# Optimization experiments

Hardware: AMD Instinct MI355X
Metric: run time of the kernel (lower is better)

The kernel has to match this reference:

```python
import jax, jax.numpy as jnp
import numpy as np

B, OBS, H, N = 16384, 512, 1024, 9

def setup_inputs() -> dict:
    key = jax.random.key(0)
    ks = jax.random.split(key, 12)
    s = 0.02
    return {
        "obs": jax.random.normal(ks[0], (B, OBS), jnp.float32),
        "agent_positions": jax.random.normal(ks[1], (B, N, 3), jnp.float32),
        "W1": jax.random.normal(ks[2], (OBS, H), jnp.float32) * s,
        "b1": jnp.zeros((H,), jnp.float32),
        "W2": jax.random.normal(ks[3], (H, H), jnp.float32) * s,
        "b2": jnp.zeros((H,), jnp.float32),
        "Wc1": jax.random.normal(ks[4], (H, H // 2), jnp.float32) * s,
        "bc1": jnp.zeros((H // 2,), jnp.float32),
        "Wc2": jax.random.normal(ks[5], (H // 2, 1), jnp.float32) * s,
        "bc2": jnp.zeros((1,), jnp.float32),
        "Wt1": jax.random.normal(ks[6], (H, H // 2), jnp.float32) * s,
        "bt1": jnp.zeros((H // 2,), jnp.float32),
        "Wt2": jax.random.normal(ks[7], (H // 2, 1), jnp.float32) * s,
        "bt2": jnp.zeros((1,), jnp.float32),
        "Wk1": jax.random.normal(ks[8], (2 * H, H), jnp.float32) * s,
        "bk1": jnp.zeros((H,), jnp.float32),
        "Wk2": jax.random.normal(ks[9], (H, 1), jnp.float32) * s,
        "bk2": jnp.zeros((1,), jnp.float32),
    }


def reference(obs, agent_positions, W1, b1, W2, b2, Wc1, bc1, Wc2, bc2,
              Wt1, bt1, Wt2, bt2, Wk1, bk1, Wk2, bk2):
    # global features: Linear->ReLU->Linear->ReLU
    g = jax.nn.relu(obs @ W1 + b1)
    g = jax.nn.relu(g @ W2 + b2)  # [B, H]

    # Each per-agent head is applied to the SAME g in the original loop,
    # so one pass + broadcast is mathematically identical.
    cov = jax.nn.sigmoid(jax.nn.relu(g @ Wc1 + bc1) @ Wc2 + bc2)  # [B,1]
    trk = jax.nn.sigmoid(jax.nn.relu(g @ Wt1 + bt1) @ Wt2 + bt2)  # [B,1]
    coop_in = jnp.concatenate([g, g], axis=-1)                    # [B,2H]
    coop = jax.nn.sigmoid(jax.nn.relu(coop_in @ Wk1 + bk1) @ Wk2 + bk2)  # [B,1]
    # mean over 8 identical cooperation scores == the score itself

    coverage = jnp.broadcast_to(cov, (cov.shape[0], N))      # [B, N]
    tracking = jnp.broadcast_to(trk, (trk.shape[0], N))      # [B, N]
    cooperation = jnp.broadcast_to(coop, (coop.shape[0], N)) # [B, N]
    return (coverage, tracking, cooperation)
```

## Files before the change

### kernel.cpp

```cpp
#include <hip/hip_runtime.h>
#include <hip/hip_bf16.h>

#define B_ROWS 16384
#define OBS_D  512
#define H_D    1024
#define N_AG   9

typedef __attribute__((ext_vector_type(8))) short short8;
typedef __attribute__((ext_vector_type(4))) float floatx4;

__device__ __forceinline__ unsigned short f_to_bf_raw(float f) {
  union { float f; unsigned u; } c; c.f = f;
  unsigned u = c.u;
  u = u + 0x7FFF + ((u >> 16) & 1);
  return (unsigned short)(u >> 16);
}

__global__ __launch_bounds__(256) void prep_all(
    const float* __restrict__ obs,
    const float* __restrict__ W1, const float* __restrict__ W2,
    const float* __restrict__ Wc1, const float* __restrict__ Wt1,
    const float* __restrict__ Wk1,
    const float* __restrict__ bc1, const float* __restrict__ bt1,
    const float* __restrict__ bk1,
    const float* __restrict__ Wc2, const float* __restrict__ Wt2,
    const float* __restrict__ Wk2,
    unsigned short* __restrict__ obs_bf,
    unsigned short* __restrict__ W1T, unsigned short* __restrict__ W2T,
    unsigned short* __restrict__ WH,
    float* __restrict__ bias2048, float* __restrict__ w2cat) {
  __shared__ float t[32][33];
  const int bx  = blockIdx.x;
  const int tid = threadIdx.x;

  if (bx < 4096) {
    int i = (bx * 256 + tid) * 8;
    float4 a = *(const float4*)(obs + i);
    float4 b = *(const float4*)(obs + i + 4);
    short8 o;
    o[0] = (short)f_to_bf_raw(a.x); o[1] = (short)f_to_bf_raw(a.y);
    o[2] = (short)f_to_bf_raw(a.z); o[3] = (short)f_to_bf_raw(a.w);
    o[4] = (short)f_to_bf_raw(b.x); o[5] = (short)f_to_bf_raw(b.y);
    o[6] = (short)f_to_bf_raw(b.z); o[7] = (short)f_to_bf_raw(b.w);
    *(short8*)(obs_bf + i) = o;
    return;
  }

  const int tx = tid & 31;
  const int ty = tid >> 5;

  if (bx < 4608) {
    const int tt = bx - 4096;
    const int k0 = (tt & 15) * 32;
    const int n0 = (tt >> 4) * 32;
#pragma unroll
    for (int i = ty; i < 32; i += 8)
      t[i][tx] = W1[(size_t)(k0 + i) * 1024 + n0 + tx];
    __syncthreads();
#pragma unroll
    for (int i = ty; i < 32; i += 8)
      W1T[(size_t)(n0 + i) * 512 + k0 + tx] = f_to_bf_raw(t[tx][i]);
    return;
  }

  if (bx < 5632) {
    const int tt = bx - 4608;
    const int k0 = (tt & 31) * 32;
    const int n0 = (tt >> 5) * 32;
#pragma unroll
    for (int i = ty; i < 32; i += 8)
      t[i][tx] = W2[(size_t)(k0 + i) * 1024 + n0 + tx];
    __syncthreads();
#pragma unroll
    for (int i = ty; i < 32; i += 8)
      W2T[(size_t)(n0 + i) * 1024 + k0 + tx] = f_to_bf_raw(t[tx][i]);
    return;
  }

  if (bx < 7680) {
    const int tt = bx - 5632;
    const int k0 = (tt & 31) * 32;
    const int n0 = (tt >> 5) * 32;
#pragma unroll
    for (int i = ty; i < 32; i += 8) {
      const int n = n0 + tx;
      float v;
      if (n0 < 512)
        v = Wc1[(size_t)(k0 + i) * 512 + n];
      else if (n0 < 1024)
        v = Wt1[(size_t)(k0 + i) * 512 + (n - 512)];
      else
        v = Wk1[(size_t)(k0 + i) * 1024 + (n - 1024)]
          + Wk1[(size_t)(k0 + i + 1024) * 1024 + (n - 1024)];
      t[i][tx] = v;
    }
    __syncthreads();
#pragma unroll
    for (int i = ty; i < 32; i += 8)
      WH[(size_t)(n0 + i) * 1024 + k0 + tx] = f_to_bf_raw(t[tx][i]);
    return;
  }

  {
    int n = (bx - 7680) * 256 + tid;
    float b, w;
    if (n < 512)       { b = bc1[n];        w = Wc2[n]; }
    else if (n < 1024) { b = bt1[n - 512];  w = Wt2[n - 512]; }
    else               { b = bk1[n - 1024]; w = Wk2[n - 1024]; }
    bias2048[n] = b;
    w2cat[n] = w;
  }
}

#define GEMM_CORE_V3(ACC_DECL)                                                 \
  __shared__ __align__(16) unsigned short As[128 * 64];                        \
  __shared__ __align__(16) unsigned short Bs[128 * 64];                        \
  const int tid  = threadIdx.x;                                                \
  const int lane = tid & 63;                                                   \
  const int wave = tid >> 6;                                                   \
  const int m0 = blockIdx.x * 128;                                             \
  const int n0 = blockIdx.y * 128;                                             \
  const int wm = (wave & 1) * 64;                                              \
  const int wn = (wave >> 1) * 64;                                             \
  const int fr = lane & 15;                                                    \
  const int fq = lane >> 4;                                                    \
  ACC_DECL;                                                                    \
  const size_t rowb = (size_t)K * 2;                                           \
  const int srow8 = lane >> 3;                \
  const int scolx = (lane & 7) ^ srow8;       \
  const char* gA = (const char*)A + (size_t)(m0 + wave * 32 + srow8) * rowb    \
                   + scolx * 16;                                               \
  const char* gB = (const char*)Bt + (size_t)(n0 + wave * 32 + srow8) * rowb   \
                   + scolx * 16;                                               \
  char* lA = (char*)As + (wave * 32) * 128 + lane * 16;                        \
  char* lB = (char*)Bs + (wave * 32) * 128 + lane * 16;                        \
  const int fsA = (wm + fr) * 128;                 \
  const int fsB = (wn + fr) * 128;                                             \
  const int fx7 = (fr & 7);                                                    \
  for (int k0 = 0; k0 < K; k0 += 64) {                                         \
    _Pragma("unroll")                                                          \
    for (int j = 0; j < 4; ++j) {                                              \
      __builtin_amdgcn_global_load_lds(                                        \
          (const __attribute__((address_space(1))) void*)(gA + (size_t)j * 8 * rowb), \
          (__attribute__((address_space(3))) void*)(lA + j * 1024), 16, 0, 0); \
      __builtin_amdgcn_global_load_lds(                                        \
          (const __attribute__((address_space(1))) void*)(gB + (size_t)j * 8 * rowb), \
          (__attribute__((address_space(3))) void*)(lB + j * 1024), 16, 0, 0); \
    }                                                                          \
    gA += 128; gB += 128;                                                      \
    __syncthreads();                                                           \
    short8 af[4][2], bf[4][2];                                                 \
    _Pragma("unroll")                                                          \
    for (int ks = 0; ks < 2; ++ks) {                                           \
      const int cA = ks * 4 + fq;                                              \
      const int slot = (cA ^ fx7) * 16;                                        \
      _Pragma("unroll")                                                        \
      for (int mi = 0; mi < 4; ++mi)                                           \
        af[mi][ks] = *(const short8*)((const char*)As + fsA + mi * 2048 + slot); \
      _Pragma("unroll")                                                        \
      for (int ni = 0; ni < 4; ++ni)                                           \
        bf[ni][ks] = *(const short8*)((const char*)Bs + fsB + ni * 2048 + slot); \
    }                                                                          \
    _Pragma("unroll")                                                          \
    for (int ks = 0; ks < 2; ++ks)                                             \
      _Pragma("unroll")                                                        \
      for (int mi = 0; mi < 4; ++mi)                                           \
        _Pragma("unroll")                                                      \
        for (int ni = 0; ni < 4; ++ni)                                         \
          acc[mi][ni] = __builtin_amdgcn_mfma_f32_16x16x32_bf16(               \
              af[mi][ks], bf[ni][ks], acc[mi][ni], 0, 0, 0);                   \
    __syncthreads();                                                           \
  }

#define ACC_INIT                                                               \
  floatx4 acc[4][4];                                                           \
  _Pragma("unroll")                                                            \
  for (int i = 0; i < 4; ++i)                                                  \
    _Pragma("unroll")                                                          \
    for (int j = 0; j < 4; ++j) acc[i][j] = (floatx4){0.f, 0.f, 0.f, 0.f}

__global__ __launch_bounds__(256) void gemm_bias_relu(
    const unsigned short* __restrict__ A,
    const unsigned short* __restrict__ Bt,
    const float* __restrict__ bias,
    unsigned short* __restrict__ C,
    int M, int N, int K) {
  GEMM_CORE_V3(ACC_INIT)

#pragma unroll
  for (int ni = 0; ni < 4; ++ni) {
    const int gn = n0 + wn + ni * 16 + fr;
    const float bv = bias[gn];
#pragma unroll
    for (int mi = 0; mi < 4; ++mi) {
#pragma unroll
      for (int r = 0; r < 4; ++r) {
        const int gm = m0 + wm + mi * 16 + fq * 4 + r;
        float v = acc[mi][ni][r] + bv;
        v = v > 0.f ? v : 0.f;
        C[(size_t)gm * N + gn] = f_to_bf_raw(v);
      }
    }
  }
}

__global__ __launch_bounds__(256) void gemm_heads_fused(
    const unsigned short* __restrict__ A,
    const unsigned short* __restrict__ Bt,
    const float* __restrict__ bias,
    const float* __restrict__ w2,
    float* __restrict__ part,
    int M, int N, int K) {
  GEMM_CORE_V3(ACC_INIT)

  const int j = blockIdx.y * 2 + (wave >> 1);
  float w2v[4], bv[4];
#pragma unroll
  for (int ni = 0; ni < 4; ++ni) {
    const int gn = n0 + wn + ni * 16 + fr;
    w2v[ni] = w2[gn];
    bv[ni]  = bias[gn];
  }
#pragma unroll
  for (int mi = 0; mi < 4; ++mi) {
#pragma unroll
    for (int r = 0; r < 4; ++r) {
      float p = 0.f;
#pragma unroll
      for (int ni = 0; ni < 4; ++ni) {
        float v = acc[mi][ni][r] + bv[ni];
        v = v > 0.f ? v : 0.f;
        p += v * w2v[ni];
      }
      p += __shfl_xor(p, 1);
      p += __shfl_xor(p, 2);
      p += __shfl_xor(p, 4);
      p += __shfl_xor(p, 8);
      if (fr == 0) {
        const int gm = m0 + wm + mi * 16 + fq * 4 + r;
        part[(size_t)j * B_ROWS + gm] = p;
      }
    }
  }
}

__global__ __launch_bounds__(256) void final_out(
    const float* __restrict__ part,
    const float* __restrict__ bc2, const float* __restrict__ bt2,
    const float* __restrict__ bk2, float* __restrict__ out) {
  const int row = blockIdx.x * 256 + threadIdx.x;
  float sc = 0.f, st = 0.f, sk = 0.f;
#pragma unroll
  for (int j = 0; j < 8; ++j)  sc += part[(size_t)j * B_ROWS + row];
#pragma unroll
  for (int j = 8; j < 16; ++j) st += part[(size_t)j * B_ROWS + row];
#pragma unroll
  for (int j = 16; j < 32; ++j) sk += part[(size_t)j * B_ROWS + row];
  const float cv = 1.f / (1.f + expf(-(sc + bc2[0])));
  const float tv = 1.f / (1.f + expf(-(st + bt2[0])));
  const float kv = 1.f / (1.f + expf(-(sk + bk2[0])));
  float* o0 = out + (size_t)row * N_AG;
  float* o1 = out + (size_t)(B_ROWS + row) * N_AG;
  float* o2 = out + (size_t)(2 * B_ROWS + row) * N_AG;
#pragma unroll
  for (int a = 0; a < N_AG; ++a) { o0[a] = cv; o1[a] = tv; o2[a] = kv; }
}

extern "C" void kernel_launch(void* const* d_in, const int* in_sizes, int n_in,
                              void* d_out, int out_size, void* d_ws, size_t ws_size,
                              hipStream_t stream) {
  const float* obs = (const float*)d_in[0];
  const float* W1  = (const float*)d_in[2];
  const float* b1  = (const float*)d_in[3];
  const float* W2  = (const float*)d_in[4];
  const float* b2  = (const float*)d_in[5];
  const float* Wc1 = (const float*)d_in[6];
  const float* bc1 = (const float*)d_in[7];
  const float* Wc2 = (const float*)d_in[8];
  const float* bc2 = (const float*)d_in[9];
  const float* Wt1 = (const float*)d_in[10];
  const float* bt1 = (const float*)d_in[11];
  const float* Wt2 = (const float*)d_in[12];
  const float* bt2 = (const float*)d_in[13];
  const float* Wk1 = (const float*)d_in[14];
  const float* bk1 = (const float*)d_in[15];
  const float* Wk2 = (const float*)d_in[16];
  const float* bk2 = (const float*)d_in[17];
  float* out = (float*)d_out;

  char* ws = (char*)d_ws;
  unsigned short* obs_bf  = (unsigned short*)(ws + 0);
  float*          PART    = (float*)(ws + 0);
  unsigned short* W1T     = (unsigned short*)(ws + 16777216);
  unsigned short* W2T     = (unsigned short*)(ws + 17825792);
  unsigned short* WH      = (unsigned short*)(ws + 19922944);
  float*          bias2048= (float*)(ws + 24117248);
  float*          w2cat   = (float*)(ws + 24125440);
  unsigned short* G1      = (unsigned short*)(ws + 24330240);
  unsigned short* G       = (unsigned short*)(ws + 57884672);

  prep_all<<<7688, 256, 0, stream>>>(obs, W1, W2, Wc1, Wt1, Wk1,
                                     bc1, bt1, bk1, Wc2, Wt2, Wk2,
                                     obs_bf, W1T, W2T, WH, bias2048, w2cat);

  gemm_bias_relu<<<dim3(128, 8), 256, 0, stream>>>(obs_bf, W1T, b1, G1, B_ROWS, 1024, 512);
  gemm_bias_relu<<<dim3(128, 8), 256, 0, stream>>>(G1, W2T, b2, G, B_ROWS, 1024, 1024);

  gemm_heads_fused<<<dim3(128, 16), 256, 0, stream>>>(G, WH, bias2048, w2cat, PART,
                                                      B_ROWS, 2048, 1024);

  final_out<<<B_ROWS / 256, 256, 0, stream>>>(PART, bc2, bt2, bk2, out);
}
```

Before: 282.4 us.

## Double-buffer LDS tiles with K-step 32 to overlap global loads with MFMA

Replaces the single-buffered 64-wide K tile GEMM core with a two-stage LDS ping-pong of 32-wide K tiles. The loads for the next tile are issued right after the barrier, before the MFMAs on the current tile, so global latency can hide behind compute, and only one barrier per iteration remains. The XOR swizzle is reworked for the narrower rows. In exchange each barrier covers only half the K work, and the loop has twice as many iterations with less MFMA work per iteration.

```diff
diff --git a/kernel.cpp b/kernel.cpp
--- a/kernel.cpp
+++ b/kernel.cpp
@@ -112,9 +112,9 @@
   }
 }
 
-#define GEMM_CORE_V3(ACC_DECL)                                                 \
-  __shared__ __align__(16) unsigned short As[128 * 64];                        \
-  __shared__ __align__(16) unsigned short Bs[128 * 64];                        \
+#define GEMM_CORE_V4(ACC_DECL)                                                 \
+  __shared__ __align__(16) unsigned short As[2][128 * 32];                     \
+  __shared__ __align__(16) unsigned short Bs[2][128 * 32];                     \
   const int tid  = threadIdx.x;                                                \
   const int lane = tid & 63;                                                   \
   const int wave = tid >> 6;                                                   \
@@ -126,50 +126,67 @@
   const int fq = lane >> 4;                                                    \
   ACC_DECL;                                                                    \
   const size_t rowb = (size_t)K * 2;                                           \
-  const int srow8 = lane >> 3;                \
-  const int scolx = (lane & 7) ^ srow8;       \
-  const char* gA = (const char*)A + (size_t)(m0 + wave * 32 + srow8) * rowb    \
-                   + scolx * 16;                                               \
-  const char* gB = (const char*)Bt + (size_t)(n0 + wave * 32 + srow8) * rowb   \
-                   + scolx * 16;                                               \
-  char* lA = (char*)As + (wave * 32) * 128 + lane * 16;                        \
-  char* lB = (char*)Bs + (wave * 32) * 128 + lane * 16;                        \
-  const int fsA = (wm + fr) * 128;                 \
-  const int fsB = (wn + fr) * 128;                                             \
-  const int fx7 = (fr & 7);                                                    \
-  for (int k0 = 0; k0 < K; k0 += 64) {                                         \
+  const int srow   = lane >> 2;                 \
+  const int schunk = (lane & 3) ^ ((srow >> 1) & 3);   \
+  const char* gA0 = (const char*)A + (size_t)(m0 + wave * 32 + srow) * rowb    \
+                    + schunk * 16;                                             \
+  const char* gA1 = gA0 + 16 * rowb;                                           \
+  const char* gB0 = (const char*)Bt + (size_t)(n0 + wave * 32 + srow) * rowb   \
+                    + schunk * 16;                                             \
+  const char* gB1 = gB0 + 16 * rowb;                                           \
+  char* lA = (char*)&As[0][0] + (wave * 32) * 64 + lane * 16;                  \
+  char* lB = (char*)&Bs[0][0] + (wave * 32) * 64 + lane * 16;                  \
+  const int fswz = (fr >> 1) & 3;                                              \
+  const int fsA = (wm + fr) * 64 + ((fq ^ fswz) * 16);                         \
+  const int fsB = (wn + fr) * 64 + ((fq ^ fswz) * 16);                         \
+  __builtin_amdgcn_global_load_lds(                                            \
+      (const __attribute__((address_space(1))) void*)gA0,                      \
+      (__attribute__((address_space(3))) void*)lA, 16, 0, 0);                  \
+  __builtin_amdgcn_global_load_lds(                                            \
+      (const __attribute__((address_space(1))) void*)gA1,                      \
+      (__attribute__((address_space(3))) void*)(lA + 1024), 16, 0, 0);         \
+  __builtin_amdgcn_global_load_lds(                                            \
+      (const __attribute__((address_space(1))) void*)gB0,                      \
+      (__attribute__((address_space(3))) void*)lB, 16, 0, 0);                  \
+  __builtin_amdgcn_global_load_lds(                                            \
+      (const __attribute__((address_space(1))) void*)gB1,                      \
+      (__attribute__((address_space(3))) void*)(lB + 1024), 16, 0, 0);         \
+  gA0 += 64; gA1 += 64; gB0 += 64; gB1 += 64;                                  \
+  for (int k0 = 0; k0 < K; k0 += 32) {                                         \
+    const int cb = (k0 >> 5) & 1;                                              \
+    __syncthreads();                                                           \
+    if (k0 + 32 < K) {                                                         \
+      char* dA = lA + (cb ^ 1) * 8192;                                         \
+      char* dB = lB + (cb ^ 1) * 8192;                                         \
+      __builtin_amdgcn_global_load_lds(                                        \
+          (const __attribute__((address_space(1))) void*)gA0,                  \
+          (__attribute__((address_space(3))) void*)dA, 16, 0, 0);              \
+      __builtin_amdgcn_global_load_lds(                                        \
+          (const __attribute__((address_space(1))) void*)gA1,                  \
+          (__attribute__((address_space(3))) void*)(dA + 1024), 16, 0, 0);     \
+      __builtin_amdgcn_global_load_lds(                                        \
+          (const __attribute__((address_space(1))) void*)gB0,                  \
+          (__attribute__((address_space(3))) void*)dB, 16, 0, 0);              \
+      __builtin_amdgcn_global_load_lds(                                        \
+          (const __attribute__((address_space(1))) void*)gB1,                  \
+          (__attribute__((address_space(3))) void*)(dB + 1024), 16, 0, 0);     \
+      gA0 += 64; gA1 += 64; gB0 += 64; gB1 += 64;                              \
+    }                                                                          \
+    const char* bAs = (const char*)&As[0][0] + cb * 8192;                      \
+    const char* bBs = (const char*)&Bs[0][0] + cb * 8192;                      \
+    short8 af[4], bf8[4];                                                      \
     _Pragma("unroll")                                                          \
-    for (int j = 0; j < 4; ++j) {                                              \
-      __builtin_amdgcn_global_load_lds(                                        \
-          (const __attribute__((address_space(1))) void*)(gA + (size_t)j * 8 * rowb), \
-          (__attribute__((address_space(3))) void*)(lA + j * 1024), 16, 0, 0); \
-      __builtin_amdgcn_global_load_lds(                                        \
-          (const __attribute__((address_space(1))) void*)(gB + (size_t)j * 8 * rowb), \
-          (__attribute__((address_space(3))) void*)(lB + j * 1024), 16, 0, 0); \
-    }                                                                          \
-    gA += 128; gB += 128;                                                      \
-    __syncthreads();                                                           \
-    short8 af[4][2], bf[4][2];                                                 \
+    for (int mi = 0; mi < 4; ++mi)                                             \
+      af[mi] = *(const short8*)(bAs + fsA + mi * 1024);                        \
     _Pragma("unroll")                                                          \
-    for (int ks = 0; ks < 2; ++ks) {                                           \
-      const int cA = ks * 4 + fq;                                              \
-      const int slot = (cA ^ fx7) * 16;                                        \
-      _Pragma("unroll")                                                        \
-      for (int mi = 0; mi < 4; ++mi)                                           \
-        af[mi][ks] = *(const short8*)((const char*)As + fsA + mi * 2048 + slot); \
+    for (int ni = 0; ni < 4; ++ni)                                             \
+      bf8[ni] = *(const short8*)(bBs + fsB + ni * 1024);                       \
+    _Pragma("unroll")                                                          \
+    for (int mi = 0; mi < 4; ++mi)                                             \
       _Pragma("unroll")                                                        \
       for (int ni = 0; ni < 4; ++ni)                                           \
-        bf[ni][ks] = *(const short8*)((const char*)Bs + fsB + ni * 2048 + slot); \
-    }                                                                          \
-    _Pragma("unroll")                                                          \
-    for (int ks = 0; ks < 2; ++ks)                                             \
-      _Pragma("unroll")                                                        \
-      for (int mi = 0; mi < 4; ++mi)                                           \
-        _Pragma("unroll")                                                      \
-        for (int ni = 0; ni < 4; ++ni)                                         \
-          acc[mi][ni] = __builtin_amdgcn_mfma_f32_16x16x32_bf16(               \
-              af[mi][ks], bf[ni][ks], acc[mi][ni], 0, 0, 0);                   \
-    __syncthreads();                                                           \
+        acc[mi][ni] = __builtin_amdgcn_mfma_f32_16x16x32_bf16(                 \
+            af[mi], bf8[ni], acc[mi][ni], 0, 0, 0);                            \
   }
 
 #define ACC_INIT                                                               \
@@ -185,7 +202,7 @@
     const float* __restrict__ bias,
     unsigned short* __restrict__ C,
     int M, int N, int K) {
-  GEMM_CORE_V3(ACC_INIT)
+  GEMM_CORE_V4(ACC_INIT)
 
 #pragma unroll
   for (int ni = 0; ni < 4; ++ni) {
@@ -211,7 +228,7 @@
     const float* __restrict__ w2,
     float* __restrict__ part,
     int M, int N, int K) {
-  GEMM_CORE_V3(ACC_INIT)
+  GEMM_CORE_V4(ACC_INIT)
 
   const int j = blockIdx.y * 2 + (wave >> 1);
   float w2v[4], bv[4];
```

Result: no change. 287.7 us (+1.8%).
